# Performance work log

Hardware: AMD Instinct MI355X
Metric: run time of the kernel (lower is better)

## Reference

```python
import jax, jax.numpy as jnp
import numpy as np

K_RATIO = 0.2
EPS = 1e-6


def setup_inputs() -> dict:
    key = jax.random.key(0)
    k1, k2 = jax.random.split(key)
    B, C, D, H, W = 2, 4, 128, 128, 128
    logits = jax.random.normal(k1, (B, C, D, H, W), dtype=jnp.float32)
    labels = jax.random.randint(k2, (B, D, H, W), 0, C)
    # one-hot target along channel axis 1, matching the tensor-path `target` arg
    target = jax.nn.one_hot(labels, C, axis=1, dtype=jnp.float32)
    return {"logits": logits, "target": target}


def reference(logits, target):
    B, C = logits.shape[0], logits.shape[1]

    # ---- Top-K cross entropy (ignore_index=-1 -> all voxels valid) ----
    y = jnp.argmax(target, axis=1)  # [B, D, H, W] int labels
    logp = jax.nn.log_softmax(logits, axis=1)
    # CE per voxel: -logp[b, y, d, h, w]
    ce = -jnp.take_along_axis(logp, y[:, None], axis=1)[:, 0]  # [B, D, H, W]
    ce_flat = ce.reshape(B, -1)  # [B, N]
    N = ce_flat.shape[1]
    k = max(1, int(N * K_RATIO))  # static: all voxels valid, k < N
    topk_vals, _ = jax.lax.top_k(ce_flat, k)  # [B, k]
    topk_loss = jnp.mean(jnp.mean(topk_vals, axis=1))

    # ---- Soft dice (no valid_mask in tensor path) ----
    p = jax.nn.softmax(logits, axis=1)  # [B, C, D, H, W]
    spatial = tuple(range(2, p.ndim))
    num = 2.0 * jnp.sum(p * target, axis=spatial)          # [B, C]
    den = jnp.sum(p + target, axis=spatial) + EPS          # [B, C]
    dice = 1.0 - num / den                                  # [B, C]
    if C > 1:
        dice = dice[:, 1:]  # drop background channel
    dice_loss = jnp.mean(dice)

    return topk_loss + 0.5 * dice_loss
```

## Files before the change

### kernel.cpp

```cpp
#include <hip/hip_runtime.h>
#include <stdint.h>

#define NVOX (1u << 21)
#define NB   2
#define KSEL 419430u
#define TPB  256
#define VPB  2048
#define BPB  ((int)(NVOX / VPB))
#define NBLK (NB * BPB)
#define NCOPY 64
#define NHC  16
#define NBINS 2048
#define SH   20
#define FIXS 262144.0f

__device__ __forceinline__ float wred64(float v) {
#pragma unroll
  for (int o = 32; o > 0; o >>= 1) v += __shfl_down(v, o, 64);
  return v;
}

__global__ __launch_bounds__(256) void k_zero(float4* __restrict__ p, int n4) {
  int i = blockIdx.x * 256 + threadIdx.x;
  if (i < n4) p[i] = make_float4(0.f, 0.f, 0.f, 0.f);
}

__global__ __launch_bounds__(TPB, 8) void k1_fused(
    const float* __restrict__ logits, const float* __restrict__ target,
    uint32_t* __restrict__ hcnt, float* __restrict__ hsum,
    float* __restrict__ dice_acc )
{
  __shared__ unsigned long long hbin[NBINS];
  const int tid = threadIdx.x;
  for (int i = tid; i < NBINS; i += TPB) hbin[i] = 0ull;
  __syncthreads();

  const int blk = blockIdx.x;
  const int b = blk / BPB;
  const size_t v0 = (size_t)(blk % BPB) * VPB;
  const float* lg = logits + (size_t)b * 4 * NVOX + v0;
  const float* tg = target + (size_t)b * 4 * NVOX + v0;

  float sp[4] = {0.f,0.f,0.f,0.f}, nm[4] = {0.f,0.f,0.f,0.f}, ct[4] = {0.f,0.f,0.f,0.f};

  for (int i = tid * 4; i < VPB; i += TPB * 4) {
    float4 L[4], T[4];
#pragma unroll
    for (int c = 0; c < 4; ++c) {
      L[c] = *(const float4*)(lg + (size_t)c * NVOX + i);
      T[c] = *(const float4*)(tg + (size_t)c * NVOX + i);
    }
#pragma unroll
    for (int j = 0; j < 4; ++j) {
      float l[4], t[4];
#pragma unroll
      for (int c = 0; c < 4; ++c) {
        l[c] = ((const float*)&L[c])[j];
        t[c] = ((const float*)&T[c])[j];
      }
      float m = fmaxf(fmaxf(l[0], l[1]), fmaxf(l[2], l[3]));
      float e[4]; float s = 0.f;
#pragma unroll
      for (int c = 0; c < 4; ++c) { e[c] = __expf(l[c] - m); s += e[c]; }
      float inv = 1.f / s;
      float lse = __logf(s);
      float ly = l[0]*t[0] + l[1]*t[1] + l[2]*t[2] + l[3]*t[3];
      float cev = (m - ly) + lse;
      uint32_t idx = __float_as_uint(cev) >> SH;
      if (idx > NBINS - 1) idx = NBINS - 1;
      unsigned long long pk = (1ull << 40) | (unsigned long long)(cev * FIXS);
      atomicAdd(&hbin[idx], pk);
#pragma unroll
      for (int c = 0; c < 4; ++c) {
        float p = e[c] * inv;
        sp[c] += p;
        nm[c] += p * t[c];
        ct[c] += t[c];
      }
    }
  }

#pragma unroll
  for (int c = 0; c < 4; ++c) { sp[c] = wred64(sp[c]); nm[c] = wred64(nm[c]); ct[c] = wred64(ct[c]); }
  if ((tid & 63) == 0) {
    float* dst = dice_acc + ((size_t)(blk & (NCOPY - 1)) * NB + b) * 12;
#pragma unroll
    for (int c = 0; c < 4; ++c) {
      atomicAdd(dst + c,     sp[c]);
      atomicAdd(dst + 4 + c, nm[c]);
      atomicAdd(dst + 8 + c, ct[c]);
    }
  }
  __syncthreads();
  const size_t hoff = ((size_t)b * NHC + (size_t)(blk & (NHC - 1))) * NBINS;
  uint32_t* cdst = hcnt + hoff;
  float*    sdst = hsum + hoff;
  for (int i = tid; i < NBINS; i += TPB) {
    unsigned long long v = hbin[i];
    if (v) {
      atomicAdd(&cdst[i], (uint32_t)(v >> 40));
      atomicAdd(&sdst[i], (float)(v & 0xFFFFFFFFFFull) * (1.0f / FIXS));
    }
  }
}

__global__ __launch_bounds__(256) void k_reduce(
    const uint32_t* __restrict__ hcnt, const float* __restrict__ hsum,
    uint32_t* __restrict__ rcnt, float* __restrict__ rsum)
{
  const int b = blockIdx.x >> 1;
  const int seg = blockIdx.x & 1;
  const int base = seg * 1024 + threadIdx.x * 4;
  uint4 c = {0,0,0,0};
  float4 s = {0.f,0.f,0.f,0.f};
  for (int copy = 0; copy < NHC; ++copy) {
    const size_t off = ((size_t)b * NHC + copy) * NBINS + base;
    uint4 cv = *(const uint4*)(hcnt + off);
    float4 sv = *(const float4*)(hsum + off);
    c.x += cv.x; c.y += cv.y; c.z += cv.z; c.w += cv.w;
    s.x += sv.x; s.y += sv.y; s.z += sv.z; s.w += sv.w;
  }
  *(uint4*)(rcnt + (size_t)b * NBINS + base) = c;
  *(float4*)(rsum + (size_t)b * NBINS + base) = s;
}

__global__ __launch_bounds__(256) void k_final(
    const uint32_t* __restrict__ rcnt, const float* __restrict__ rsum,
    const float* __restrict__ dice_acc, float* __restrict__ out)
{
  __shared__ uint32_t shc[NBINS];
  __shared__ uint32_t chunk[256];
  __shared__ uint32_t sbkt, srem;
  __shared__ float wpart[4];
  __shared__ float ts[NB];
  __shared__ float comp[24];
  const int tid = threadIdx.x;

  for (int b = 0; b < NB; ++b) {
    const uint32_t* rc = rcnt + (size_t)b * NBINS;
    const float*    rs = rsum + (size_t)b * NBINS;
    uint32_t s = 0;
#pragma unroll
    for (int q = 0; q < 2; ++q) {
      uint4 v = *(const uint4*)(rc + tid * 8 + q * 4);
      *(uint4*)&shc[tid * 8 + q * 4] = v;
      s += v.x + v.y + v.z + v.w;
    }
    chunk[tid] = s;
    __syncthreads();
    if (tid == 0) {
      uint32_t k = KSEL, cum = 0;
      int ci = 255;
      for (; ci > 0; --ci) {
        uint32_t c = chunk[ci];
        if (cum + c >= k) break;
        cum += c;
      }
      int bkt = ci * 8;
      for (int j = 7; j >= 0; --j) {
        uint32_t c = shc[ci * 8 + j];
        if (cum + c >= k) { bkt = ci * 8 + j; break; }
        cum += c;
      }
      sbkt = (uint32_t)bkt;
      srem = k - cum;
    }
    __syncthreads();
    const int bkt = (int)sbkt;
    float w = 0.f;
#pragma unroll
    for (int j = 0; j < 8; ++j) {
      int bin = tid * 8 + j;
      if (bin > bkt) w += rs[bin];
    }
    w = wred64(w);
    if ((tid & 63) == 0) wpart[tid >> 6] = w;
    __syncthreads();
    if (tid == 0) {
      float cnt_t = (float)shc[bkt];
      float sum_t = rs[bkt];
      float lo = __uint_as_float((uint32_t)bkt << SH);
      float hi = __uint_as_float((uint32_t)(bkt + 1) << SH);
      float width = hi - lo;
      float avg = sum_t / cnt_t;
      float frac = (float)srem / cnt_t;
      float est = avg + (1.f - frac) * 0.5f * width;
      ts[b] = wpart[0] + wpart[1] + wpart[2] + wpart[3] + (float)srem * est;
    }
    __syncthreads();
  }

  if (tid < 24) {
    float a = 0.f;
    for (int r = 0; r < NCOPY; ++r) a += dice_acc[(size_t)r * 24 + tid];
    comp[tid] = a;
  }
  __syncthreads();
  if (tid == 0) {
    float dl = 0.f;
#pragma unroll
    for (int b = 0; b < 2; ++b)
#pragma unroll
      for (int c = 1; c < 4; ++c) {
        float sp = comp[b * 12 + c];
        float nm = comp[b * 12 + 4 + c];
        float ct = comp[b * 12 + 8 + c];
        dl += 1.f - (2.f * nm) / (sp + ct + 1e-6f);
      }
    float topk = 0.5f * (ts[0] + ts[1]) / (float)KSEL;
    out[0] = topk + 0.5f * (dl / 6.f);
  }
}

extern "C" void kernel_launch(void* const* d_in, const int* in_sizes, int n_in,
                              void* d_out, int out_size, void* d_ws, size_t ws_size,
                              hipStream_t stream) {
  (void)in_sizes; (void)n_in; (void)out_size; (void)ws_size;
  const float* logits = (const float*)d_in[0];
  const float* target = (const float*)d_in[1];
  float* out = (float*)d_out;

  char* ws = (char*)d_ws;
  uint32_t* hcnt = (uint32_t*)ws;
  float*    hsum = (float*)(hcnt + (size_t)NB * NHC * NBINS);
  float*    dice_acc = hsum + (size_t)NB * NHC * NBINS;
  uint32_t* rcnt = (uint32_t*)(dice_acc + (size_t)NCOPY * NB * 12);
  float*    rsum = (float*)(rcnt + (size_t)NB * NBINS);
  const size_t ZERO_BYTES = (size_t)((char*)(dice_acc + (size_t)NCOPY * NB * 12) - ws);
  const int n4 = (int)(ZERO_BYTES / 16);

  k_zero<<<(n4 + 255) / 256, 256, 0, stream>>>((float4*)ws, n4);
  k1_fused<<<NBLK, TPB, 0, stream>>>(logits, target, hcnt, hsum, dice_acc);
  k_reduce<<<NB * 2, 256, 0, stream>>>(hcnt, hsum, rcnt, rsum);
  k_final<<<1, 256, 0, stream>>>(rcnt, rsum, dice_acc, out);
}
```

Measured before the change: 185.1 us.

## Replace global atomic histogram merge with per-block partials and tree reduce

Each block now writes its full 64-bit packed shared histogram and its per-block dice partials straight to global memory, with no global atomics. A 64-block reduce kernel sums the packed count/fixed-point fields in integer form, and the final kernel reduces all per-block dice partials. This removes the zero-fill kernel and the atomic contention on 16 histogram copies. The block size doubles to 4096 voxels to halve the partial count, with a partially unrolled loop. The cost is about 16 MB of histogram writes and reads (1024 blocks × 2048 × 8 bytes), which may rival the atomic cost it replaces.

```diff
diff --git a/kernel.cpp b/kernel.cpp
--- a/kernel.cpp
+++ b/kernel.cpp
@@ -5,32 +5,28 @@
 #define NB   2
 #define KSEL 419430u
 #define TPB  256
-#define VPB  2048
+#define VPB  4096
 #define BPB  ((int)(NVOX / VPB))
 #define NBLK (NB * BPB)
-#define NCOPY 64
-#define NHC  16
 #define NBINS 2048
 #define SH   20
 #define FIXS 262144.0f
 
+typedef unsigned long long u64;
+
 __device__ __forceinline__ float wred64(float v) {
 #pragma unroll
   for (int o = 32; o > 0; o >>= 1) v += __shfl_down(v, o, 64);
   return v;
 }
 
-__global__ __launch_bounds__(256) void k_zero(float4* __restrict__ p, int n4) {
-  int i = blockIdx.x * 256 + threadIdx.x;
-  if (i < n4) p[i] = make_float4(0.f, 0.f, 0.f, 0.f);
-}
-
-__global__ __launch_bounds__(TPB, 8) void k1_fused(
+__global__ __launch_bounds__(TPB, 4) void k1_fused(
     const float* __restrict__ logits, const float* __restrict__ target,
-    uint32_t* __restrict__ hcnt, float* __restrict__ hsum,
-    float* __restrict__ dice_acc )
+    u64* __restrict__ hist ,
+    float* __restrict__ dice )
 {
-  __shared__ unsigned long long hbin[NBINS];
+  __shared__ u64 hbin[NBINS];
+  __shared__ float dsh[4][12];
   const int tid = threadIdx.x;
   for (int i = tid; i < NBINS; i += TPB) hbin[i] = 0ull;
   __syncthreads();
@@ -43,6 +39,7 @@
 
   float sp[4] = {0.f,0.f,0.f,0.f}, nm[4] = {0.f,0.f,0.f,0.f}, ct[4] = {0.f,0.f,0.f,0.f};
 
+#pragma unroll 2
   for (int i = tid * 4; i < VPB; i += TPB * 4) {
     float4 L[4], T[4];
 #pragma unroll
@@ -67,8 +64,8 @@
       float ly = l[0]*t[0] + l[1]*t[1] + l[2]*t[2] + l[3]*t[3];
       float cev = (m - ly) + lse;
       uint32_t idx = __float_as_uint(cev) >> SH;
-      if (idx > NBINS - 1) idx = NBINS - 1;
-      unsigned long long pk = (1ull << 40) | (unsigned long long)(cev * FIXS);
+      idx = min(idx, (uint32_t)(NBINS - 1));
+      u64 pk = (1ull << 40) | (u64)(cev * FIXS);
       atomicAdd(&hbin[idx], pk);
 #pragma unroll
       for (int c = 0; c < 4; ++c) {
@@ -83,57 +80,61 @@
 #pragma unroll
   for (int c = 0; c < 4; ++c) { sp[c] = wred64(sp[c]); nm[c] = wred64(nm[c]); ct[c] = wred64(ct[c]); }
   if ((tid & 63) == 0) {
-    float* dst = dice_acc + ((size_t)(blk & (NCOPY - 1)) * NB + b) * 12;
+    const int w = tid >> 6;
 #pragma unroll
     for (int c = 0; c < 4; ++c) {
-      atomicAdd(dst + c,     sp[c]);
-      atomicAdd(dst + 4 + c, nm[c]);
-      atomicAdd(dst + 8 + c, ct[c]);
-    }
-  }
-  __syncthreads();
-  const size_t hoff = ((size_t)b * NHC + (size_t)(blk & (NHC - 1))) * NBINS;
-  uint32_t* cdst = hcnt + hoff;
-  float*    sdst = hsum + hoff;
-  for (int i = tid; i < NBINS; i += TPB) {
-    unsigned long long v = hbin[i];
-    if (v) {
-      atomicAdd(&cdst[i], (uint32_t)(v >> 40));
-      atomicAdd(&sdst[i], (float)(v & 0xFFFFFFFFFFull) * (1.0f / FIXS));
-    }
-  }
+      dsh[w][c]     = sp[c];
+      dsh[w][4 + c] = nm[c];
+      dsh[w][8 + c] = ct[c];
+    }
+  }
+  __syncthreads();
+  if (tid < 12)
+    dice[(size_t)blk * 12 + tid] = dsh[0][tid] + dsh[1][tid] + dsh[2][tid] + dsh[3][tid];
+
+  u64* hdst = hist + (size_t)blk * NBINS;
+  for (int i = tid; i < NBINS; i += TPB) hdst[i] = hbin[i];
 }
 
 __global__ __launch_bounds__(256) void k_reduce(
-    const uint32_t* __restrict__ hcnt, const float* __restrict__ hsum,
-    uint32_t* __restrict__ rcnt, float* __restrict__ rsum)
+    const u64* __restrict__ hist, uint32_t* __restrict__ rcnt,
+    float* __restrict__ rsum)
 {
-  const int b = blockIdx.x >> 1;
-  const int seg = blockIdx.x & 1;
-  const int base = seg * 1024 + threadIdx.x * 4;
-  uint4 c = {0,0,0,0};
-  float4 s = {0.f,0.f,0.f,0.f};
-  for (int copy = 0; copy < NHC; ++copy) {
-    const size_t off = ((size_t)b * NHC + copy) * NBINS + base;
-    uint4 cv = *(const uint4*)(hcnt + off);
-    float4 sv = *(const float4*)(hsum + off);
-    c.x += cv.x; c.y += cv.y; c.z += cv.z; c.w += cv.w;
-    s.x += sv.x; s.y += sv.y; s.z += sv.z; s.w += sv.w;
-  }
-  *(uint4*)(rcnt + (size_t)b * NBINS + base) = c;
-  *(float4*)(rsum + (size_t)b * NBINS + base) = s;
+  const int e = blockIdx.x;
+  const int b = e >> 5;
+  const int seg = e & 31;
+  const int lane = threadIdx.x & 63;
+  const int wave = threadIdx.x >> 6;
+  const int bin = seg * 64 + lane;
+  const u64* base = hist + (size_t)b * BPB * NBINS + bin;
+  u64 csum = 0, fsum = 0;
+  const int r0 = wave * (BPB / 4), r1 = r0 + BPB / 4;
+  for (int r = r0; r < r1; ++r) {
+    u64 v = base[(size_t)r * NBINS];
+    csum += v >> 40;
+    fsum += v & 0xFFFFFFFFFFull;
+  }
+  __shared__ u64 sc[4][64], ss[4][64];
+  sc[wave][lane] = csum; ss[wave][lane] = fsum;
+  __syncthreads();
+  if (wave == 0) {
+    csum = sc[0][lane] + sc[1][lane] + sc[2][lane] + sc[3][lane];
+    fsum = ss[0][lane] + ss[1][lane] + ss[2][lane] + ss[3][lane];
+    rcnt[b * NBINS + bin] = (uint32_t)csum;
+    rsum[b * NBINS + bin] = (float)((double)fsum * (1.0 / 262144.0));
+  }
 }
 
 __global__ __launch_bounds__(256) void k_final(
     const uint32_t* __restrict__ rcnt, const float* __restrict__ rsum,
-    const float* __restrict__ dice_acc, float* __restrict__ out)
+    const float* __restrict__ dice, float* __restrict__ out)
 {
   __shared__ uint32_t shc[NBINS];
   __shared__ uint32_t chunk[256];
   __shared__ uint32_t sbkt, srem;
   __shared__ float wpart[4];
   __shared__ float ts[NB];
-  __shared__ float comp[24];
+  __shared__ float cpart[4][24];
   const int tid = threadIdx.x;
 
   for (int b = 0; b < NB; ++b) {
@@ -190,13 +191,32 @@
     __syncthreads();
   }
 
-  if (tid < 24) {
-    float a = 0.f;
-    for (int r = 0; r < NCOPY; ++r) a += dice_acc[(size_t)r * 24 + tid];
-    comp[tid] = a;
+  float a0[12], a1[12];
+#pragma unroll
+  for (int c = 0; c < 12; ++c) { a0[c] = 0.f; a1[c] = 0.f; }
+  for (int r = tid; r < NBLK; r += 256) {
+    const float* dp = dice + (size_t)r * 12;
+    if (r < BPB) {
+#pragma unroll
+      for (int c = 0; c < 12; ++c) a0[c] += dp[c];
+    } else {
+#pragma unroll
+      for (int c = 0; c < 12; ++c) a1[c] += dp[c];
+    }
+  }
+#pragma unroll
+  for (int c = 0; c < 12; ++c) { a0[c] = wred64(a0[c]); a1[c] = wred64(a1[c]); }
+  if ((tid & 63) == 0) {
+    const int w = tid >> 6;
+#pragma unroll
+    for (int c = 0; c < 12; ++c) { cpart[w][c] = a0[c]; cpart[w][12 + c] = a1[c]; }
   }
   __syncthreads();
   if (tid == 0) {
+    float comp[24];
+#pragma unroll
+    for (int c = 0; c < 24; ++c)
+      comp[c] = cpart[0][c] + cpart[1][c] + cpart[2][c] + cpart[3][c];
     float dl = 0.f;
 #pragma unroll
     for (int b = 0; b < 2; ++b)
@@ -221,16 +241,12 @@
   float* out = (float*)d_out;
 
   char* ws = (char*)d_ws;
-  uint32_t* hcnt = (uint32_t*)ws;
-  float*    hsum = (float*)(hcnt + (size_t)NB * NHC * NBINS);
-  float*    dice_acc = hsum + (size_t)NB * NHC * NBINS;
-  uint32_t* rcnt = (uint32_t*)(dice_acc + (size_t)NCOPY * NB * 12);
+  u64*      hist = (u64*)ws;
+  float*    dice = (float*)(hist + (size_t)NBLK * NBINS);
+  uint32_t* rcnt = (uint32_t*)(dice + (size_t)NBLK * 12);
   float*    rsum = (float*)(rcnt + (size_t)NB * NBINS);
-  const size_t ZERO_BYTES = (size_t)((char*)(dice_acc + (size_t)NCOPY * NB * 12) - ws);
-  const int n4 = (int)(ZERO_BYTES / 16);
-
-  k_zero<<<(n4 + 255) / 256, 256, 0, stream>>>((float4*)ws, n4);
-  k1_fused<<<NBLK, TPB, 0, stream>>>(logits, target, hcnt, hsum, dice_acc);
-  k_reduce<<<NB * 2, 256, 0, stream>>>(hcnt, hsum, rcnt, rsum);
-  k_final<<<1, 256, 0, stream>>>(rcnt, rsum, dice_acc, out);
-}
+
+  k1_fused<<<NBLK, TPB, 0, stream>>>(logits, target, hist, dice);
+  k_reduce<<<64, 256, 0, stream>>>(hist, rcnt, rsum);
+  k_final<<<1, 256, 0, stream>>>(rcnt, rsum, dice, out);
+}
```

Measured after the change: 179.9 us. 1.03x faster.
